# Kernel optimization log

Hardware: AMD Instinct MI355X
Metric: run time of the kernel (lower is better)

## Reference

```python
import jax, jax.numpy as jnp
import numpy as np

N_PATCHES = 14
PS = 32                      # patch size = 448 // 14
HIDDEN = 64
N_HEADS = 4
DH = HIDDEN // N_HEADS       # 16
N_BLOCKS = 2
INPUT_D = PS * PS            # c=1 -> 1024
MLP_R = 4
EPS = 1e-5                   # nn.LayerNorm default


def _pos_emb(S, d):
    # get_positional_embeddings: sin(i/10000**(j/d)) for even j, cos(i/10000**((j-1)/d)) for odd j
    i = jnp.arange(S, dtype=jnp.float32)[:, None]
    j = jnp.arange(d, dtype=jnp.float32)[None, :]
    even = (jnp.arange(d) % 2 == 0)[None, :]
    ae = i / jnp.power(jnp.float32(10000.0), j / d)
    ao = i / jnp.power(jnp.float32(10000.0), (j - 1.0) / d)
    return jnp.where(even, jnp.sin(ae), jnp.cos(ao))


def _patchify(images):
    # [n,c,h,w] -> [n, n_patches^2, c*ps*ps]; patch flattened in (c, row, col) order as in torch .flatten()
    n, c, h, w = images.shape
    x = images.reshape(n, c, N_PATCHES, PS, N_PATCHES, PS)
    x = x.transpose(0, 2, 4, 1, 3, 5)            # [n, pi, pj, c, ps, ps]
    return x.reshape(n, N_PATCHES * N_PATCHES, c * PS * PS)


def _depatchify(p):
    # inverse of _patchify with c=1 (as the original depatchify derives c = np2/n_patches^2 = 1)
    n = p.shape[0]
    x = p.reshape(n, N_PATCHES, N_PATCHES, 1, PS, PS)
    x = x.transpose(0, 3, 1, 4, 2, 5)
    return x.reshape(n, 1, N_PATCHES * PS, N_PATCHES * PS)


def _ln(x, g, b):
    m = x.mean(-1, keepdims=True)
    v = ((x - m) ** 2).mean(-1, keepdims=True)
    return (x - m) / jnp.sqrt(v + EPS) * g + b


def _msa(x, Wq, bq, Wk, bk, Wv, bv):
    # batched over sequences and heads; equivalent to the original per-seq/per-head python loops
    n, S, d = x.shape
    xh = x.reshape(n, S, N_HEADS, DH)
    q = jnp.einsum('nshd,hde->nshe', xh, Wq) + bq
    k = jnp.einsum('nshd,hde->nshe', xh, Wk) + bk
    v = jnp.einsum('nshd,hde->nshe', xh, Wv) + bv
    att = jax.nn.softmax(jnp.einsum('nshe,nthe->nhst', q, k) / jnp.sqrt(jnp.float32(DH)), axis=-1)
    o = jnp.einsum('nhst,nthe->nshe', att, v)    # [n,S,h,dh]
    return o.reshape(n, S, d)                    # hstack over heads == contiguous head layout


def _block(x, p, i):
    h = x + _msa(_ln(x, p['ln1_g'][i], p['ln1_b'][i]),
                 p['Wq'][i], p['bq'][i], p['Wk'][i], p['bk'][i], p['Wv'][i], p['bv'][i])
    z = _ln(h, p['ln2_g'][i], p['ln2_b'][i])
    z = jax.nn.gelu(z @ p['W1'][i] + p['b1'][i], approximate=False) @ p['W2'][i] + p['b2'][i]
    return h + z


def setup_inputs() -> dict:
    key = jax.random.key(0)
    ks = iter(jax.random.split(key, 80))
    def rn(shape, s=0.02):
        return jax.random.normal(next(ks), shape, dtype=jnp.float32) * s
    N = 128
    inp = {
        'images': jax.random.normal(next(ks), (N, 1, 448, 448), dtype=jnp.float32),
        'class_token': jax.random.uniform(next(ks), (1, HIDDEN), dtype=jnp.float32),  # torch.rand init
        'lm_W': rn((INPUT_D, HIDDEN)), 'lm_b': jnp.zeros((HIDDEN,), jnp.float32),
        'lm2_W': rn((HIDDEN, INPUT_D)), 'lm2_b': jnp.zeros((INPUT_D,), jnp.float32),
        'mlp1_W': rn((HIDDEN, 1)), 'mlp1_b': jnp.zeros((1,), jnp.float32),
        'mlp4_W': rn((1, HIDDEN)), 'mlp4_b': jnp.zeros((HIDDEN,), jnp.float32),
    }
    for pre in ('enc_', 'dec_'):
        inp[pre + 'ln1_g'] = jnp.ones((N_BLOCKS, HIDDEN), jnp.float32)
        inp[pre + 'ln1_b'] = jnp.zeros((N_BLOCKS, HIDDEN), jnp.float32)
        inp[pre + 'ln2_g'] = jnp.ones((N_BLOCKS, HIDDEN), jnp.float32)
        inp[pre + 'ln2_b'] = jnp.zeros((N_BLOCKS, HIDDEN), jnp.float32)
        for nm in ('Wq', 'Wk', 'Wv'):
            inp[pre + nm] = rn((N_BLOCKS, N_HEADS, DH, DH), 0.05)
        for nm in ('bq', 'bk', 'bv'):
            inp[pre + nm] = jnp.zeros((N_BLOCKS, N_HEADS, DH), jnp.float32)
        inp[pre + 'W1'] = rn((N_BLOCKS, HIDDEN, MLP_R * HIDDEN))
        inp[pre + 'b1'] = jnp.zeros((N_BLOCKS, MLP_R * HIDDEN), jnp.float32)
        inp[pre + 'W2'] = rn((N_BLOCKS, MLP_R * HIDDEN, HIDDEN))
        inp[pre + 'b2'] = jnp.zeros((N_BLOCKS, HIDDEN), jnp.float32)
    return inp


def reference(images, class_token, lm_W, lm_b, lm2_W, lm2_b,
              mlp1_W, mlp1_b, mlp4_W, mlp4_b,
              enc_ln1_g, enc_ln1_b, enc_ln2_g, enc_ln2_b,
              enc_Wq, enc_bq, enc_Wk, enc_bk, enc_Wv, enc_bv,
              enc_W1, enc_b1, enc_W2, enc_b2,
              dec_ln1_g, dec_ln1_b, dec_ln2_g, dec_ln2_b,
              dec_Wq, dec_bq, dec_Wk, dec_bk, dec_Wv, dec_bv,
              dec_W1, dec_b1, dec_W2, dec_b2):
    n = images.shape[0]
    patches = _patchify(images)                            # [n, 196, 1024]
    tokens = patches @ lm_W + lm_b                         # [n, 196, 64]
    cls = jnp.broadcast_to(class_token[None], (n, 1, HIDDEN))
    out = jnp.concatenate([cls, tokens], axis=1)           # [n, 197, 64]
    out = out + _pos_emb(N_PATCHES ** 2 + 1, HIDDEN)[None]
    enc = dict(ln1_g=enc_ln1_g, ln1_b=enc_ln1_b, ln2_g=enc_ln2_g, ln2_b=enc_ln2_b,
               Wq=enc_Wq, bq=enc_bq, Wk=enc_Wk, bk=enc_bk, Wv=enc_Wv, bv=enc_bv,
               W1=enc_W1, b1=enc_b1, W2=enc_W2, b2=enc_b2)
    for i in range(N_BLOCKS):
        out = _block(out, enc, i)
    lat = jax.nn.gelu(out[:, 1:, :] @ mlp1_W + mlp1_b, approximate=False)   # [n, 196, 1]
    out = jax.nn.gelu(lat @ mlp4_W + mlp4_b, approximate=False)             # [n, 196, 64]
    dec = dict(ln1_g=dec_ln1_g, ln1_b=dec_ln1_b, ln2_g=dec_ln2_g, ln2_b=dec_ln2_b,
               Wq=dec_Wq, bq=dec_bq, Wk=dec_Wk, bk=dec_bk, Wv=dec_Wv, bv=dec_bv,
               W1=dec_W1, b1=dec_b1, W2=dec_W2, b2=dec_b2)
    for i in range(N_BLOCKS):
        out = _block(out, dec, i)
    out = out + _pos_emb(N_PATCHES ** 2, HIDDEN)[None]
    out = out @ lm2_W + lm2_b                              # [n, 196, 1024]
    reimage = _depatchify(out)                             # [n, 1, 448, 448]
    return (lat, reimage)
```

## Files before the change

kernel.cpp:

```cpp
#include <hip/hip_runtime.h>
#include <math.h>

#define N_IMG 128
#define EPS 1e-5f
#define PART_STRIDE 1614848

__device__ __forceinline__ float gelu_f(float x) {
    return 0.5f * x * (1.0f + erff(x * 0.70710678118654752f));
}

__device__ __forceinline__ float wave_sum(float v) {
    #pragma unroll
    for (int m = 1; m < 64; m <<= 1) v += __shfl_xor(v, m);
    return v;
}

__device__ __forceinline__ void fma4(float4& acc, float s, const float4& v) {
    acc.x += s * v.x; acc.y += s * v.y; acc.z += s * v.z; acc.w += s * v.w;
}

__device__ __forceinline__ float dot4(const float4& a, const float4& b) {
    return a.x * b.x + a.y * b.y + a.z * b.z + a.w * b.w;
}

__global__ void k_posemb(float* __restrict__ pe) {
    int idx = blockIdx.x * 256 + threadIdx.x;
    if (idx >= 197 * 64) return;
    int i = idx >> 6, j = idx & 63;
    int jj = j & ~1;
    float inv = powf(10000.0f, (float)jj / 64.0f);
    float a = (float)i / inv;
    pe[idx] = (j & 1) ? cosf(a) : sinf(a);
}

__global__ __launch_bounds__(256, 6) void k_patch(
    const float* __restrict__ img, const float* __restrict__ W,
    float* __restrict__ part)
{
    __shared__ float As[64 * 44];
    __shared__ float Bs[32 * 76];
    int tid = threadIdx.x;
    int tx = tid & 15, ty = tid >> 4;
    int m0 = blockIdx.x * 64;
    int kc0 = blockIdx.y * 8;

    int ra = tid >> 2, ca = (tid & 3) * 8;
    int rowa = m0 + ra;
    int na = rowa / 196, pa = rowa - na * 196;
    const float* abase = img + (size_t)na * 200704 + (pa / 14) * (32 * 448) + (pa % 14) * 32 + ca;

    int kr = tid >> 3, cb = (tid & 7) * 8;

    float4 acc[4];
    #pragma unroll
    for (int i = 0; i < 4; ++i) acc[i] = make_float4(0.f, 0.f, 0.f, 0.f);

    for (int it = 0; it < 8; ++it) {
        int kc = kc0 + it;
        float4 a0 = *(const float4*)(abase + kc * 448);
        float4 a1 = *(const float4*)(abase + kc * 448 + 4);
        const float* wp = W + (size_t)(kc * 32 + kr) * 64 + cb;
        float4 b0 = *(const float4*)(wp);
        float4 b1 = *(const float4*)(wp + 4);
        __syncthreads();
        *(float4*)&As[ra * 44 + ca]     = a0;
        *(float4*)&As[ra * 44 + ca + 4] = a1;
        *(float4*)&Bs[kr * 76 + cb]     = b0;
        *(float4*)&Bs[kr * 76 + cb + 4] = b1;
        __syncthreads();
        #pragma unroll 4
        for (int k4 = 0; k4 < 8; ++k4) {
            float4 a[4], b[4];
            #pragma unroll
            for (int i = 0; i < 4; ++i) a[i] = *(float4*)&As[(ty + 16 * i) * 44 + k4 * 4];
            #pragma unroll
            for (int kk = 0; kk < 4; ++kk) b[kk] = *(float4*)&Bs[(k4 * 4 + kk) * 76 + tx * 4];
            #pragma unroll
            for (int i = 0; i < 4; ++i) {
                fma4(acc[i], a[i].x, b[0]);
                fma4(acc[i], a[i].y, b[1]);
                fma4(acc[i], a[i].z, b[2]);
                fma4(acc[i], a[i].w, b[3]);
            }
        }
    }
    float* pp = part + (size_t)blockIdx.y * PART_STRIDE;
    int col = tx * 4;
    #pragma unroll
    for (int i = 0; i < 4; ++i) {
        int row = m0 + ty + 16 * i;
        *(float4*)&pp[(size_t)row * 64 + col] = acc[i];
    }
}

__global__ __launch_bounds__(256) void k_pcomb(
    const float* __restrict__ part, const float* __restrict__ bias,
    const float* __restrict__ pe, float* __restrict__ x)
{
    int idx = blockIdx.x * 256 + threadIdx.x;
    int row = idx >> 4, c4 = (idx & 15) * 4;
    int n = row / 196, p = row - n * 196;
    const float* p0 = part + (size_t)row * 64 + c4;
    float4 a = *(const float4*)(p0);
    float4 b = *(const float4*)(p0 + PART_STRIDE);
    float4 c = *(const float4*)(p0 + 2 * (size_t)PART_STRIDE);
    float4 d = *(const float4*)(p0 + 3 * (size_t)PART_STRIDE);
    float4 bb = *(const float4*)(bias + c4);
    float4 pv = *(const float4*)(pe + (size_t)(1 + p) * 64 + c4);
    float4 o;
    o.x = a.x + b.x + c.x + d.x + bb.x + pv.x;
    o.y = a.y + b.y + c.y + d.y + bb.y + pv.y;
    o.z = a.z + b.z + c.z + d.z + bb.z + pv.z;
    o.w = a.w + b.w + c.w + d.w + bb.w + pv.w;
    *(float4*)&x[((size_t)(n * 197 + 1 + p)) * 64 + c4] = o;
}

__global__ void k_cls(const float* __restrict__ cls, const float* __restrict__ pe,
                      float* __restrict__ x) {
    int idx = blockIdx.x * 256 + threadIdx.x;
    if (idx >= 128 * 64) return;
    int n = idx >> 6, j = idx & 63;
    x[(size_t)n * 197 * 64 + j] = cls[j] + pe[j];
}

__global__ __launch_bounds__(256, 2) void k_ln_qkv(
    const float* __restrict__ x, const float* __restrict__ g, const float* __restrict__ bta,
    const float* __restrict__ Wq, const float* __restrict__ bq,
    const float* __restrict__ Wk, const float* __restrict__ bk,
    const float* __restrict__ Wv, const float* __restrict__ bv,
    float* __restrict__ q, float* __restrict__ k, float* __restrict__ v, int S)
{
    __shared__ float z[4][64];
    int tid = threadIdx.x, w = tid >> 6, l = tid & 63;
    int row = blockIdx.x * 4 + w;
    if (row >= N_IMG * S) return;
    float xv = x[(size_t)row * 64 + l];
    float m = wave_sum(xv) * (1.0f / 64.0f);
    float t = xv - m;
    float var = wave_sum(t * t) * (1.0f / 64.0f);
    float zv = t * rsqrtf(var + EPS) * g[l] + bta[l];
    z[w][l] = zv;
    int h = l >> 4, e = l & 15;
    const float* zh = &z[w][h * 16];
    const float* wq = Wq + h * 256 + e;
    const float* wk = Wk + h * 256 + e;
    const float* wv = Wv + h * 256 + e;
    float aq = bq[l], ak = bk[l], av = bv[l];
    #pragma unroll
    for (int d = 0; d < 16; ++d) {
        float zd = zh[d];
        aq += zd * wq[d * 16];
        ak += zd * wk[d * 16];
        av += zd * wv[d * 16];
    }
    int n = row / S, s = row - n * S;
    size_t o = ((size_t)((n * 4 + h) * S + s)) * 16 + e;
    q[o] = aq; k[o] = ak; v[o] = av;
}

struct KV { float4 k[2][4]; float4 v[2][4]; };

__device__ __forceinline__ void ld_pair(KV& b, const float* kp, const float* vp, int j) {
    #pragma unroll
    for (int u = 0; u < 2; ++u) {
        #pragma unroll
        for (int c = 0; c < 4; ++c) {
            b.k[u][c] = *(const float4*)(kp + (size_t)(j + u) * 16 + c * 4);
            b.v[u][c] = *(const float4*)(vp + (size_t)(j + u) * 16 + c * 4);
        }
    }
}

__device__ __forceinline__ void comp_one(const KV& b, int u, const float4* qv,
                                         float& l, float4* o) {
    float sc = dot4(qv[0], b.k[u][0]) + dot4(qv[1], b.k[u][1]) +
               dot4(qv[2], b.k[u][2]) + dot4(qv[3], b.k[u][3]);
    float p = __expf(sc);
    l += p;
    fma4(o[0], p, b.v[u][0]); fma4(o[1], p, b.v[u][1]);
    fma4(o[2], p, b.v[u][2]); fma4(o[3], p, b.v[u][3]);
}

__global__ __launch_bounds__(256, 2) void k_attn(
    const float* __restrict__ q, const float* __restrict__ k, const float* __restrict__ v,
    const float* __restrict__ x, float* __restrict__ hout, int S)
{
    int h = blockIdx.x & 3, n = blockIdx.x >> 2;
    int tid = threadIdx.x;
    int s = tid < S ? tid : S - 1;
    const float* qrow = q + ((size_t)((n * 4 + h) * S + s)) * 16;
    float4 qv[4];
    #pragma unroll
    for (int c = 0; c < 4; ++c) {
        float4 t = *(const float4*)(qrow + c * 4);
        t.x *= 0.25f; t.y *= 0.25f; t.z *= 0.25f; t.w *= 0.25f;
        qv[c] = t;
    }
    const float* kp = k + (size_t)(n * 4 + h) * S * 16;
    const float* vp = v + (size_t)(n * 4 + h) * S * 16;
    float l = 0.0f;
    float4 o[4];
    #pragma unroll
    for (int c = 0; c < 4; ++c) o[c] = make_float4(0.f, 0.f, 0.f, 0.f);

    KV A, B;
    ld_pair(A, kp, vp, 0);
    int j = 0;
    for (; j + 4 <= S; j += 4) {
        ld_pair(B, kp, vp, j + 2);
        comp_one(A, 0, qv, l, o);
        comp_one(A, 1, qv, l, o);
        ld_pair(A, kp, vp, j + 4);
        comp_one(B, 0, qv, l, o);
        comp_one(B, 1, qv, l, o);
    }
    int rem = S - j;
    if (rem > 0) comp_one(A, 0, qv, l, o);
    if (rem > 1) comp_one(A, 1, qv, l, o);
    if (rem > 2) {
        ld_pair(B, kp, vp, j + 2);
        comp_one(B, 0, qv, l, o);
    }

    float rl = 1.0f / l;
    if (tid < S) {
        size_t base = ((size_t)n * S + tid) * 64 + h * 16;
        #pragma unroll
        for (int e4 = 0; e4 < 4; ++e4) {
            float4 xv = *(const float4*)(x + base + e4 * 4);
            float4 w;
            w.x = xv.x + o[e4].x * rl;
            w.y = xv.y + o[e4].y * rl;
            w.z = xv.z + o[e4].z * rl;
            w.w = xv.w + o[e4].w * rl;
            *(float4*)(hout + base + e4 * 4) = w;
        }
    }
}

__global__ __launch_bounds__(256, 4) void k_mlp1(
    const float* __restrict__ hbuf, const float* __restrict__ g, const float* __restrict__ bta,
    const float* __restrict__ W1, const float* __restrict__ b1,
    float* __restrict__ mid)
{
    __shared__ float As[64 * 76];
    __shared__ float Bs[64 * 76];
    int tid = threadIdx.x;
    int tx = tid & 15, ty = tid >> 4;
    int m0 = blockIdx.x * 64;
    int nc = blockIdx.y;
    int r = tid >> 2, cpart = (tid & 3) * 16;
    {
        const float* hp = hbuf + ((size_t)(m0 + r)) * 64 + cpart;
        float4 hv[4];
        #pragma unroll
        for (int i = 0; i < 4; ++i) hv[i] = *(const float4*)(hp + i * 4);
        float ps = 0.f;
        #pragma unroll
        for (int i = 0; i < 4; ++i) ps += hv[i].x + hv[i].y + hv[i].z + hv[i].w;
        ps += __shfl_xor(ps, 1); ps += __shfl_xor(ps, 2);
        float mean = ps * (1.0f / 64.0f);
        float vs = 0.f;
        #pragma unroll
        for (int i = 0; i < 4; ++i) {
            float dx = hv[i].x - mean, dy = hv[i].y - mean, dz = hv[i].z - mean, dw = hv[i].w - mean;
            vs += dx * dx + dy * dy + dz * dz + dw * dw;
        }
        vs += __shfl_xor(vs, 1); vs += __shfl_xor(vs, 2);
        float rstd = rsqrtf(vs * (1.0f / 64.0f) + EPS);
        #pragma unroll
        for (int i = 0; i < 4; ++i) {
            float4 gv = *(const float4*)(g + cpart + i * 4);
            float4 bv = *(const float4*)(bta + cpart + i * 4);
            float4 zv;
            zv.x = (hv[i].x - mean) * rstd * gv.x + bv.x;
            zv.y = (hv[i].y - mean) * rstd * gv.y + bv.y;
            zv.z = (hv[i].z - mean) * rstd * gv.z + bv.z;
            zv.w = (hv[i].w - mean) * rstd * gv.w + bv.w;
            *(float4*)&As[r * 76 + cpart + i * 4] = zv;
        }
    }
    const float* wp = W1 + (size_t)r * 256 + nc * 64 + cpart;
    float4 wv4[4];
    #pragma unroll
    for (int i = 0; i < 4; ++i) wv4[i] = *(const float4*)(wp + i * 4);
    __syncthreads();
    #pragma unroll
    for (int i = 0; i < 4; ++i)
        *(float4*)&Bs[r * 76 + cpart + i * 4] = wv4[i];
    __syncthreads();
    float4 acc[4];
    #pragma unroll
    for (int i = 0; i < 4; ++i) acc[i] = make_float4(0.f, 0.f, 0.f, 0.f);
    #pragma unroll 4
    for (int k4 = 0; k4 < 16; ++k4) {
        float4 a[4], b[4];
        #pragma unroll
        for (int i = 0; i < 4; ++i) a[i] = *(float4*)&As[(ty + 16 * i) * 76 + k4 * 4];
        #pragma unroll
        for (int kk = 0; kk < 4; ++kk) b[kk] = *(float4*)&Bs[(k4 * 4 + kk) * 76 + tx * 4];
        #pragma unroll
        for (int i = 0; i < 4; ++i) {
            fma4(acc[i], a[i].x, b[0]);
            fma4(acc[i], a[i].y, b[1]);
            fma4(acc[i], a[i].z, b[2]);
            fma4(acc[i], a[i].w, b[3]);
        }
    }
    int col = nc * 64 + tx * 4;
    float4 b1v = *(const float4*)(b1 + col);
    #pragma unroll
    for (int i = 0; i < 4; ++i) {
        int row = m0 + ty + 16 * i;
        float4 ov;
        ov.x = gelu_f(acc[i].x + b1v.x);
        ov.y = gelu_f(acc[i].y + b1v.y);
        ov.z = gelu_f(acc[i].z + b1v.z);
        ov.w = gelu_f(acc[i].w + b1v.w);
        *(float4*)&mid[(size_t)row * 256 + col] = ov;
    }
}

__global__ __launch_bounds__(256, 4) void k_mlp2(
    const float* __restrict__ mid, const float* __restrict__ W2, const float* __restrict__ b2,
    const float* __restrict__ hbuf, float* __restrict__ out)
{
    __shared__ float As[32 * 76];
    __shared__ float Bs[64 * 76];
    int tid = threadIdx.x;
    int tx = tid & 15, ty = tid >> 4;
    int m0 = blockIdx.x * 32;
    int ra = tid >> 3, ca = (tid & 7) * 8;
    int rb = tid >> 2, cb = (tid & 3) * 16;
    float4 acc[2];
    acc[0] = make_float4(0.f, 0.f, 0.f, 0.f);
    acc[1] = make_float4(0.f, 0.f, 0.f, 0.f);
    for (int kc = 0; kc < 4; ++kc) {
        const float* mp = mid + ((size_t)(m0 + ra)) * 256 + kc * 64 + ca;
        float4 av0 = *(const float4*)(mp);
        float4 av1 = *(const float4*)(mp + 4);
        const float* wp = W2 + (size_t)(kc * 64 + rb) * 64 + cb;
        float4 wv4[4];
        #pragma unroll
        for (int i = 0; i < 4; ++i) wv4[i] = *(const float4*)(wp + i * 4);
        __syncthreads();
        *(float4*)&As[ra * 76 + ca]     = av0;
        *(float4*)&As[ra * 76 + ca + 4] = av1;
        #pragma unroll
        for (int i = 0; i < 4; ++i)
            *(float4*)&Bs[rb * 76 + cb + i * 4] = wv4[i];
        __syncthreads();
        #pragma unroll 4
        for (int k4 = 0; k4 < 16; ++k4) {
            float4 a[2], b[4];
            a[0] = *(float4*)&As[ty * 76 + k4 * 4];
            a[1] = *(float4*)&As[(ty + 16) * 76 + k4 * 4];
            #pragma unroll
            for (int kk = 0; kk < 4; ++kk) b[kk] = *(float4*)&Bs[(k4 * 4 + kk) * 76 + tx * 4];
            #pragma unroll
            for (int i = 0; i < 2; ++i) {
                fma4(acc[i], a[i].x, b[0]);
                fma4(acc[i], a[i].y, b[1]);
                fma4(acc[i], a[i].z, b[2]);
                fma4(acc[i], a[i].w, b[3]);
            }
        }
    }
    int col = tx * 4;
    float4 b2v = *(const float4*)(b2 + col);
    #pragma unroll
    for (int i = 0; i < 2; ++i) {
        int row = m0 + ty + 16 * i;
        float4 hv = *(const float4*)(hbuf + (size_t)row * 64 + col);
        float4 ov;
        ov.x = acc[i].x + b2v.x + hv.x;
        ov.y = acc[i].y + b2v.y + hv.y;
        ov.z = acc[i].z + b2v.z + hv.z;
        ov.w = acc[i].w + b2v.w + hv.w;
        *(float4*)&out[(size_t)row * 64 + col] = ov;
    }
}

__global__ __launch_bounds__(256) void k_bneck(
    const float* __restrict__ xenc, const float* __restrict__ m1W, const float* __restrict__ m1b,
    const float* __restrict__ m4W, const float* __restrict__ m4b,
    float* __restrict__ lat_out, float* __restrict__ xdec)
{
    int tid = threadIdx.x, w = tid >> 6, l = tid & 63;
    int row = blockIdx.x * 4 + w;
    if (row >= 128 * 196) return;
    int n = row / 196, p = row - n * 196;
    float xv = xenc[((size_t)(n * 197 + 1 + p)) * 64 + l];
    float sum = wave_sum(xv * m1W[l]);
    float lat = gelu_f(sum + m1b[0]);
    if (l == 0) lat_out[row] = lat;
    float ov = gelu_f(lat * m4W[l] + m4b[l]);
    xdec[(size_t)row * 64 + l] = ov;
}

__global__ __launch_bounds__(256, 4) void k_final(
    const float* __restrict__ xdec, const float* __restrict__ pe,
    const float* __restrict__ W, const float* __restrict__ bias,
    float* __restrict__ img_out)
{
    __shared__ float As[64 * 76];
    __shared__ float Bs[64 * 76];
    int tid = threadIdx.x;
    int tx = tid & 15, ty = tid >> 4;
    int m0 = blockIdx.x * 64;
    int r = tid >> 2, cpart = (tid & 3) * 16;
    {
        int row = m0 + r;
        int n = row / 196, p = row - n * 196;
        const float* xp = xdec + (size_t)row * 64 + cpart;
        const float* pp = pe + (size_t)p * 64 + cpart;
        #pragma unroll
        for (int i = 0; i < 4; ++i) {
            float4 xv = *(const float4*)(xp + i * 4);
            float4 pv = *(const float4*)(pp + i * 4);
            float4 zv;
            zv.x = xv.x + pv.x; zv.y = xv.y + pv.y; zv.z = xv.z + pv.z; zv.w = xv.w + pv.w;
            *(float4*)&As[r * 76 + cpart + i * 4] = zv;
        }
    }
    for (int t = 0; t < 4; ++t) {
        int nb = blockIdx.y * 4 + t;
        const float* wp = W + (size_t)r * 1024 + nb * 64 + cpart;
        float4 wv4[4];
        #pragma unroll
        for (int i = 0; i < 4; ++i) wv4[i] = *(const float4*)(wp + i * 4);
        __syncthreads();
        #pragma unroll
        for (int i = 0; i < 4; ++i)
            *(float4*)&Bs[r * 76 + cpart + i * 4] = wv4[i];
        __syncthreads();
        float4 acc[4];
        #pragma unroll
        for (int i = 0; i < 4; ++i) acc[i] = make_float4(0.f, 0.f, 0.f, 0.f);
        #pragma unroll 4
        for (int k4 = 0; k4 < 16; ++k4) {
            float4 a[4], b[4];
            #pragma unroll
            for (int i = 0; i < 4; ++i) a[i] = *(float4*)&As[(ty + 16 * i) * 76 + k4 * 4];
            #pragma unroll
            for (int kk = 0; kk < 4; ++kk) b[kk] = *(float4*)&Bs[(k4 * 4 + kk) * 76 + tx * 4];
            #pragma unroll
            for (int i = 0; i < 4; ++i) {
                fma4(acc[i], a[i].x, b[0]);
                fma4(acc[i], a[i].y, b[1]);
                fma4(acc[i], a[i].z, b[2]);
                fma4(acc[i], a[i].w, b[3]);
            }
        }
        int colj = nb * 64 + tx * 4;
        float4 bv = *(const float4*)(bias + colj);
        int rr = colj >> 5, cc = colj & 31;
        #pragma unroll
        for (int i = 0; i < 4; ++i) {
            int row = m0 + ty + 16 * i;
            int n = row / 196, p = row - n * 196;
            int pi = p / 14, pj = p - pi * 14;
            size_t off = (size_t)n * 200704 + (size_t)(pi * 32 + rr) * 448 + pj * 32 + cc;
            float4 ov;
            ov.x = acc[i].x + bv.x;
            ov.y = acc[i].y + bv.y;
            ov.z = acc[i].z + bv.z;
            ov.w = acc[i].w + bv.w;
            *(float4*)&img_out[off] = ov;
        }
    }
}

extern "C" void kernel_launch(void* const* d_in, const int* in_sizes, int n_in,
                              void* d_out, int out_size, void* d_ws, size_t ws_size,
                              hipStream_t stream) {
    const float* images = (const float*)d_in[0];
    const float* cls    = (const float*)d_in[1];
    const float* lm_W   = (const float*)d_in[2];
    const float* lm_b   = (const float*)d_in[3];
    const float* lm2_W  = (const float*)d_in[4];
    const float* lm2_b  = (const float*)d_in[5];
    const float* m1W    = (const float*)d_in[6];
    const float* m1b    = (const float*)d_in[7];
    const float* m4W    = (const float*)d_in[8];
    const float* m4b    = (const float*)d_in[9];

    float* pe   = (float*)d_ws;
    float* xb   = pe + 12608;
    float* hb   = xb + 1614848;
    float* qb   = hb + 1614848;
    float* kb   = qb + 1614848;
    float* vb   = kb + 1614848;
    float* midb = vb + 1614848;

    float* lat_out = (float*)d_out;
    float* img_out = (float*)d_out + 25088;

    hipLaunchKernelGGL(k_posemb, dim3(50), dim3(256), 0, stream, pe);
    hipLaunchKernelGGL(k_patch, dim3(392, 4), dim3(256), 0, stream, images, lm_W, qb);
    hipLaunchKernelGGL(k_pcomb, dim3(1568), dim3(256), 0, stream, qb, lm_b, pe, xb);
    hipLaunchKernelGGL(k_cls, dim3(32), dim3(256), 0, stream, cls, pe, xb);

    float* cur_x = xb;
    float* cur_h = hb;
    for (int grp = 0; grp < 2; ++grp) {
        int base = 10 + grp * 14;
        const float* ln1_g = (const float*)d_in[base + 0];
        const float* ln1_b = (const float*)d_in[base + 1];
        const float* ln2_g = (const float*)d_in[base + 2];
        const float* ln2_b = (const float*)d_in[base + 3];
        const float* Wq = (const float*)d_in[base + 4];
        const float* Wk = (const float*)d_in[base + 5];
        const float* Wv = (const float*)d_in[base + 6];
        const float* bq = (const float*)d_in[base + 7];
        const float* bk = (const float*)d_in[base + 8];
        const float* bv = (const float*)d_in[base + 9];
        const float* W1 = (const float*)d_in[base + 10];
        const float* b1 = (const float*)d_in[base + 11];
        const float* W2 = (const float*)d_in[base + 12];
        const float* b2 = (const float*)d_in[base + 13];
        int S = (grp == 0) ? 197 : 196;
        int rows = 128 * S;
        for (int i = 0; i < 2; ++i) {
            hipLaunchKernelGGL(k_ln_qkv, dim3(rows / 4), dim3(256), 0, stream,
                cur_x, ln1_g + i * 64, ln1_b + i * 64,
                Wq + i * 1024, bq + i * 64, Wk + i * 1024, bk + i * 64,
                Wv + i * 1024, bv + i * 64, qb, kb, vb, S);
            hipLaunchKernelGGL(k_attn, dim3(512), dim3(256), 0, stream,
                qb, kb, vb, cur_x, cur_h, S);
            hipLaunchKernelGGL(k_mlp1, dim3(rows / 64, 4), dim3(256), 0, stream,
                cur_h, ln2_g + i * 64, ln2_b + i * 64, W1 + i * 16384, b1 + i * 256, midb);
            hipLaunchKernelGGL(k_mlp2, dim3(rows / 32), dim3(256), 0, stream,
                midb, W2 + i * 16384, b2 + i * 64, cur_h, cur_x);
        }
        if (grp == 0) {
            hipLaunchKernelGGL(k_bneck, dim3(6272), dim3(256), 0, stream,
                cur_x, m1W, m1b, m4W, m4b, lat_out, hb);
            cur_x = hb;
            cur_h = xb;
        }
    }
    hipLaunchKernelGGL(k_final, dim3(392, 4), dim3(256), 0, stream, cur_x, pe, lm2_W, lm2_b, img_out);
}
```

Baseline: 874.6 us.

## Split attention over four key chunks and combine partial sums in a second kernel

Attention is split along the key dimension into four chunks, each handled by a separate block that writes unnormalized partial outputs and partial exp-sums into scratch space. A new combine kernel adds the partials, normalizes, and applies the residual. The aim is more blocks and shorter serial loops per thread to fill the GPU better. The cost is an extra launch and extra global traffic through the midb and img_out scratch buffers. Skipping max-subtraction is safe here only because the chunks share no running max.

```diff
diff --git a/kernel.cpp b/kernel.cpp
--- a/kernel.cpp
+++ b/kernel.cpp
@@ -4,6 +4,8 @@
 #define N_IMG 128
 #define EPS 1e-5f
 #define PART_STRIDE 1614848
+#define OP_STRIDE 1613824
+#define LP_STRIDE 100864
 
 __device__ __forceinline__ float gelu_f(float x) {
     return 0.5f * x * (1.0f + erff(x * 0.70710678118654752f));
@@ -181,11 +183,15 @@
     fma4(o[2], p, b.v[u][2]); fma4(o[3], p, b.v[u][3]);
 }
 
-__global__ __launch_bounds__(256, 2) void k_attn(
+__global__ __launch_bounds__(256, 8) void k_attn_part(
     const float* __restrict__ q, const float* __restrict__ k, const float* __restrict__ v,
-    const float* __restrict__ x, float* __restrict__ hout, int S)
+    float* __restrict__ o_part, float* __restrict__ l_part, int S)
 {
     int h = blockIdx.x & 3, n = blockIdx.x >> 2;
+    int ks = blockIdx.y;
+    int per = (S + 3) >> 2;
+    int start = ks * per;
+    int len = S - start; if (len > per) len = per;
     int tid = threadIdx.x;
     int s = tid < S ? tid : S - 1;
     const float* qrow = q + ((size_t)((n * 4 + h) * S + s)) * 16;
@@ -196,8 +202,8 @@
         t.x *= 0.25f; t.y *= 0.25f; t.z *= 0.25f; t.w *= 0.25f;
         qv[c] = t;
     }
-    const float* kp = k + (size_t)(n * 4 + h) * S * 16;
-    const float* vp = v + (size_t)(n * 4 + h) * S * 16;
+    const float* kp = k + ((size_t)(n * 4 + h) * S + start) * 16;
+    const float* vp = v + ((size_t)(n * 4 + h) * S + start) * 16;
     float l = 0.0f;
     float4 o[4];
     #pragma unroll
@@ -206,7 +212,7 @@
     KV A, B;
     ld_pair(A, kp, vp, 0);
     int j = 0;
-    for (; j + 4 <= S; j += 4) {
+    for (; j + 4 <= len; j += 4) {
         ld_pair(B, kp, vp, j + 2);
         comp_one(A, 0, qv, l, o);
         comp_one(A, 1, qv, l, o);
@@ -214,7 +220,7 @@
         comp_one(B, 0, qv, l, o);
         comp_one(B, 1, qv, l, o);
     }
-    int rem = S - j;
+    int rem = len - j;
     if (rem > 0) comp_one(A, 0, qv, l, o);
     if (rem > 1) comp_one(A, 1, qv, l, o);
     if (rem > 2) {
@@ -222,20 +228,39 @@
         comp_one(B, 0, qv, l, o);
     }
 
+    if (tid < S) {
+        size_t qlin = (size_t)(n * 4 + h) * S + tid;
+        float* op = o_part + (size_t)ks * OP_STRIDE + qlin * 16;
+        #pragma unroll
+        for (int c = 0; c < 4; ++c) *(float4*)(op + c * 4) = o[c];
+        l_part[(size_t)ks * LP_STRIDE + qlin] = l;
+    }
+}
+
+__global__ __launch_bounds__(256) void k_attn_comb(
+    const float* __restrict__ o_part, const float* __restrict__ l_part,
+    const float* __restrict__ x, float* __restrict__ hout, int S)
+{
+    int idx = blockIdx.x * 256 + threadIdx.x;
+    int qlin = idx >> 2, c4 = (idx & 3) << 2;
+    int nh = qlin / S, s = qlin - nh * S;
+    int n = nh >> 2, h = nh & 3;
+    const float* op = o_part + (size_t)qlin * 16 + c4;
+    float4 a = *(const float4*)(op);
+    float4 b = *(const float4*)(op + OP_STRIDE);
+    float4 c = *(const float4*)(op + 2 * (size_t)OP_STRIDE);
+    float4 d = *(const float4*)(op + 3 * (size_t)OP_STRIDE);
+    float l = l_part[qlin] + l_part[qlin + LP_STRIDE] +
+              l_part[qlin + 2 * LP_STRIDE] + l_part[qlin + 3 * LP_STRIDE];
     float rl = 1.0f / l;
-    if (tid < S) {
-        size_t base = ((size_t)n * S + tid) * 64 + h * 16;
-        #pragma unroll
-        for (int e4 = 0; e4 < 4; ++e4) {
-            float4 xv = *(const float4*)(x + base + e4 * 4);
-            float4 w;
-            w.x = xv.x + o[e4].x * rl;
-            w.y = xv.y + o[e4].y * rl;
-            w.z = xv.z + o[e4].z * rl;
-            w.w = xv.w + o[e4].w * rl;
-            *(float4*)(hout + base + e4 * 4) = w;
-        }
-    }
+    size_t base = ((size_t)(n * S + s)) * 64 + h * 16 + c4;
+    float4 xv = *(const float4*)(x + base);
+    float4 w;
+    w.x = xv.x + (a.x + b.x + c.x + d.x) * rl;
+    w.y = xv.y + (a.y + b.y + c.y + d.y) * rl;
+    w.z = xv.z + (a.z + b.z + c.z + d.z) * rl;
+    w.w = xv.w + (a.w + b.w + c.w + d.w) * rl;
+    *(float4*)(hout + base) = w;
 }
 
 __global__ __launch_bounds__(256, 4) void k_mlp1(
@@ -526,8 +551,10 @@
                 cur_x, ln1_g + i * 64, ln1_b + i * 64,
                 Wq + i * 1024, bq + i * 64, Wk + i * 1024, bk + i * 64,
                 Wv + i * 1024, bv + i * 64, qb, kb, vb, S);
-            hipLaunchKernelGGL(k_attn, dim3(512), dim3(256), 0, stream,
-                qb, kb, vb, cur_x, cur_h, S);
+            hipLaunchKernelGGL(k_attn_part, dim3(512, 4), dim3(256), 0, stream,
+                qb, kb, vb, midb, img_out, S);
+            hipLaunchKernelGGL(k_attn_comb, dim3(8 * S), dim3(256), 0, stream,
+                midb, img_out, cur_x, cur_h, S);
             hipLaunchKernelGGL(k_mlp1, dim3(rows / 64, 4), dim3(256), 0, stream,
                 cur_h, ln2_g + i * 64, ln2_b + i * 64, W1 + i * 16384, b1 + i * 256, midb);
             hipLaunchKernelGGL(k_mlp2, dim3(rows / 32), dim3(256), 0, stream,
```

Result: faster. 819.4 us (-6.3%).
